# Performance work log

Measured on AMD Instinct MI355X. Metric: run time of the kernel, lower is better.

The kernel has to match this reference:

```python
import jax, jax.numpy as jnp
import numpy as np

N_NODES = 100000


def setup_inputs() -> dict:
    key = jax.random.key(0)
    k1, k2, k3, k4, k5 = jax.random.split(key, 5)
    feature = jax.random.normal(k1, (N_NODES, 64), dtype=jnp.float32)
    src = jax.random.randint(k2, (1600000,), 0, N_NODES, dtype=jnp.int64)
    dst = jax.random.randint(k3, (1600000,), 0, N_NODES, dtype=jnp.int64)
    W = jax.random.normal(k4, (64, 64), dtype=jnp.float32) * 0.1  # [in_feats, out_feats]
    b = jax.random.normal(k5, (64,), dtype=jnp.float32) * 0.1
    return {"feature": feature, "src": src, "dst": dst, "W": W, "b": b}


def reference(feature, src, dst, W, b):
    # message: m_e = h[src_e]; reduce: mean over mailbox per dst node.
    msgs = feature[src]                                   # [E, d] gather
    summed = jax.ops.segment_sum(msgs, dst, num_segments=N_NODES)  # [N, d]
    ones = jnp.ones((dst.shape[0],), dtype=feature.dtype)
    deg = jax.ops.segment_sum(ones, dst, num_segments=N_NODES)    # [N]
    mean = summed / jnp.maximum(deg, 1.0)[:, None]
    # DGL: nodes with no incoming messages keep their original feature
    h = jnp.where((deg > 0)[:, None], mean, feature)
    # apply_nodes: ReLU(W h + b)
    out = jax.nn.relu(h @ W + b)
    return out
```

## Files before the change

kernel.cpp:

```cpp
#include <hip/hip_runtime.h>
#include <hip/hip_bf16.h>

#define D 64
#define LOGB 7
#define BNODES 128
#define GRP6 32
#define CH6 1024
#define TN 64

__device__ __forceinline__ float blo(unsigned u) { return __uint_as_float(u << 16); }
__device__ __forceinline__ float bhi(unsigned u) { return __uint_as_float(u & 0xffff0000u); }
__device__ __forceinline__ ushort f2bfr(float x) {
    __hip_bfloat16 hb = __float2bfloat16(x);
    return *reinterpret_cast<ushort*>(&hb);
}


__global__ __launch_bounds__(256) void k_hist(
    const int* __restrict__ dst, int* __restrict__ cnt, int n_edges, int nbkt)
{
    __shared__ int sc[1024];
    int t = threadIdx.x;
    for (int i = t; i < 1024; i += 256) sc[i] = 0;
    __syncthreads();
    int n4 = n_edges >> 2;
    const int4* d4 = (const int4*)dst;
    int stride = gridDim.x * 256;
    for (int i = blockIdx.x * 256 + t; i < n4; i += stride) {
        int4 d = d4[i];
        atomicAdd(&sc[d.x >> LOGB], 1);
        atomicAdd(&sc[d.y >> LOGB], 1);
        atomicAdd(&sc[d.z >> LOGB], 1);
        atomicAdd(&sc[d.w >> LOGB], 1);
    }
    if (blockIdx.x == 0 && t == 0)
        for (int e = n4 << 2; e < n_edges; ++e) atomicAdd(&cnt[dst[e] >> LOGB], 1);
    __syncthreads();
    for (int i = t; i < nbkt; i += 256) {
        int c = sc[i];
        if (c) atomicAdd(&cnt[i], c);
    }
}


__global__ __launch_bounds__(1024) void k_bin_scan(
    const int* __restrict__ cnt, int* __restrict__ base,
    int* __restrict__ cursor, int nbkt)
{
    int t = threadIdx.x;
    int v = (t < nbkt) ? cnt[t] : 0;
    int lane = t & 63;
    int incl = v;
    #pragma unroll
    for (int o = 1; o < 64; o <<= 1) {
        int u = __shfl_up(incl, o, 64);
        if (lane >= o) incl += u;
    }
    __shared__ int wtot[16];
    if (lane == 63) wtot[t >> 6] = incl;
    __syncthreads();
    int wpre = 0;
    int w = t >> 6;
    for (int i = 0; i < w; ++i) wpre += wtot[i];
    int excl = wpre + incl - v;
    if (t < nbkt) { base[t] = excl; cursor[t] = excl; }
    if (t == nbkt - 1) base[nbkt] = excl + v;
}


__global__ __launch_bounds__(256) void k_fused(
    const int* __restrict__ src, const int* __restrict__ dst,
    int* __restrict__ cursor, unsigned* __restrict__ packed,
    int n_edges, int sbits, int nblk,
    const float* __restrict__ feat, const float* __restrict__ W,
    ushort* __restrict__ g, int n_nodes)
{
    __shared__ __align__(16) char smem[45072];
    int t = threadIdx.x;

    if ((int)blockIdx.x < nblk) {
        int* s_cnt  = (int*)smem;
        int* s_base = (int*)(smem + 4096);
        int* s_gb   = (int*)(smem + 8192);
        int* wtot   = (int*)(smem + 12288);
        unsigned* s_stage = (unsigned*)(smem + 12304);
        int* s_addr = (int*)(smem + 28688);

        int chbase = blockIdx.x * 4096;
        int count = n_edges - chbase;
        if (count > 4096) count = 4096;

        for (int i = t; i < 1024; i += 256) s_cnt[i] = 0;
        __syncthreads();

        #pragma unroll
        for (int k = 0; k < 16; ++k) {
            int i = t + k * 256;
            if (i < count) atomicAdd(&s_cnt[dst[chbase + i] >> LOGB], 1);
        }
        __syncthreads();

        int b4 = t * 4;
        int v0 = s_cnt[b4], v1 = s_cnt[b4 + 1], v2 = s_cnt[b4 + 2], v3 = s_cnt[b4 + 3];
        int ssum = v0 + v1 + v2 + v3;
        int lane = t & 63;
        int incl = ssum;
        #pragma unroll
        for (int o = 1; o < 64; o <<= 1) {
            int u = __shfl_up(incl, o, 64);
            if (lane >= o) incl += u;
        }
        if (lane == 63) wtot[t >> 6] = incl;
        __syncthreads();
        int wpre = 0;
        int w = t >> 6;
        for (int i = 0; i < w; ++i) wpre += wtot[i];
        int excl = wpre + incl - ssum;
        s_base[b4]     = excl;
        s_base[b4 + 1] = excl + v0;
        s_base[b4 + 2] = excl + v0 + v1;
        s_base[b4 + 3] = excl + v0 + v1 + v2;
        __syncthreads();

        for (int i = t; i < 1024; i += 256) {
            int c = s_cnt[i];
            s_gb[i] = c ? atomicAdd(&cursor[i], c) : 0;
        }
        __syncthreads();
        for (int i = t; i < 1024; i += 256) s_cnt[i] = s_base[i];
        __syncthreads();

        #pragma unroll
        for (int k = 0; k < 16; ++k) {
            int i = t + k * 256;
            if (i < count) {
                int e = chbase + i;
                int d = dst[e];
                int s = src[e];
                int bkt = d >> LOGB;
                int pos = atomicAdd(&s_cnt[bkt], 1);
                s_stage[pos] = ((unsigned)(d & (BNODES - 1)) << sbits) | (unsigned)s;
                s_addr[pos]  = s_gb[bkt] + (pos - s_base[bkt]);
            }
        }
        __syncthreads();

        #pragma unroll
        for (int k = 0; k < 16; ++k) {
            int i = t + k * 256;
            if (i < count) packed[s_addr[i]] = s_stage[i];
        }
    } else {
        float* ft = (float*)smem;
        float* Ws = (float*)(smem + 16384);

        int bid = blockIdx.x - nblk;
        int n0 = bid * TN;

        if (bid == 0 && t < 64) g[(size_t)n_nodes * D + t] = 0;

        {
            const float4* W4 = (const float4*)W;
            float4* Ws4 = (float4*)Ws;
            #pragma unroll
            for (int i = 0; i < 4; ++i) Ws4[t + i * 256] = W4[t + i * 256];
        }
        {
            const float4* f4 = (const float4*)feat;
            #pragma unroll
            for (int it = 0; it < 4; ++it) {
                int i = it * 256 + t;
                int r = i >> 4, c = i & 15;
                int node = n0 + r;
                float4 v = (node < n_nodes) ? f4[(size_t)node * 16 + c]
                                            : make_float4(0.f, 0.f, 0.f, 0.f);
                ft[(4 * c + 0) * TN + r] = v.x;
                ft[(4 * c + 1) * TN + r] = v.y;
                ft[(4 * c + 2) * TN + r] = v.z;
                ft[(4 * c + 3) * TN + r] = v.w;
            }
        }
        __syncthreads();

        int nq = t >> 4, cq = t & 15;
        int n4 = nq * 4, c4 = cq * 4;

        float4 a0 = make_float4(0.f, 0.f, 0.f, 0.f);
        float4 a1 = a0, a2 = a0, a3 = a0;

        #pragma unroll 16
        for (int k = 0; k < D; ++k) {
            float4 fv = *reinterpret_cast<const float4*>(&ft[k * TN + n4]);
            float4 wv = *reinterpret_cast<const float4*>(&Ws[k * D + c4]);
            a0.x = fmaf(fv.x, wv.x, a0.x); a0.y = fmaf(fv.x, wv.y, a0.y);
            a0.z = fmaf(fv.x, wv.z, a0.z); a0.w = fmaf(fv.x, wv.w, a0.w);
            a1.x = fmaf(fv.y, wv.x, a1.x); a1.y = fmaf(fv.y, wv.y, a1.y);
            a1.z = fmaf(fv.y, wv.z, a1.z); a1.w = fmaf(fv.y, wv.w, a1.w);
            a2.x = fmaf(fv.z, wv.x, a2.x); a2.y = fmaf(fv.z, wv.y, a2.y);
            a2.z = fmaf(fv.z, wv.z, a2.z); a2.w = fmaf(fv.z, wv.w, a2.w);
            a3.x = fmaf(fv.w, wv.x, a3.x); a3.y = fmaf(fv.w, wv.y, a3.y);
            a3.z = fmaf(fv.w, wv.z, a3.z); a3.w = fmaf(fv.w, wv.w, a3.w);
        }

        float4 accs[4] = {a0, a1, a2, a3};
        #pragma unroll
        for (int i = 0; i < 4; ++i) {
            int node = n0 + n4 + i;
            if (node < n_nodes) {
                ushort4 o;
                o.x = f2bfr(accs[i].x);
                o.y = f2bfr(accs[i].y);
                o.z = f2bfr(accs[i].z);
                o.w = f2bfr(accs[i].w);
                *reinterpret_cast<ushort4*>(g + (size_t)node * D + c4) = o;
            }
        }
    }
}


__global__ __launch_bounds__(256) void k_sort128(
    const unsigned* __restrict__ packed,
    const int* __restrict__ bbase,
    int* __restrict__ csr2,
    int* __restrict__ noff,
    int n_nodes, int sbits)
{
    __shared__ int s_cnt[BNODES];
    __shared__ int s_off[BNODES + 1];

    int t = threadIdx.x;
    int b = blockIdx.x;
    int gb = bbase[b], cnt = bbase[b + 1] - gb;

    if (t < BNODES) s_cnt[t] = 0;
    __syncthreads();
    for (int i = t; i < cnt; i += 256)
        atomicAdd(&s_cnt[packed[gb + i] >> sbits], 1);
    __syncthreads();

    if (t < 64) {
        int v0 = s_cnt[2 * t], v1 = s_cnt[2 * t + 1];
        int s = v0 + v1, incl = s;
        #pragma unroll
        for (int o = 1; o < 64; o <<= 1) {
            int u = __shfl_up(incl, o, 64);
            if (t >= o) incl += u;
        }
        int excl = incl - s;
        s_off[2 * t] = excl;
        s_off[2 * t + 1] = excl + v0;
        if (t == 63) s_off[BNODES] = incl;
    }
    __syncthreads();

    if (t <= BNODES) {
        int node = b * BNODES + t;
        if (node <= n_nodes) noff[node] = gb + s_off[t];
    }
    if (t < BNODES) s_cnt[t] = s_off[t];
    __syncthreads();

    unsigned smask = (1u << sbits) - 1u;
    for (int i = t; i < cnt; i += 256) {
        unsigned v = packed[gb + i];
        int pos = atomicAdd(&s_cnt[v >> sbits], 1);
        csr2[gb + pos] = (int)(v & smask);
    }
}


__global__ __launch_bounds__(256) void k_bucket6(
    const ushort* __restrict__ g,
    const float* __restrict__ bias,
    const int* __restrict__ noff,
    const int* __restrict__ csr2,
    float* __restrict__ out, int n_nodes)
{
    __shared__ int s_src[CH6];
    __shared__ int s_noff[GRP6 + 1];

    int t = threadIdx.x;
    int n0 = blockIdx.x * GRP6;
    if (t <= GRP6) {
        int node = n0 + t;
        s_noff[t] = noff[node > n_nodes ? n_nodes : node];
    }
    __syncthreads();

    int lane = t & 63, wid = t >> 6;
    int q = lane >> 4;
    int m = lane & 15;
    const ushort* gm = g + 4 * m;

    float4 acc[8];
    #pragma unroll
    for (int k = 0; k < 8; ++k) acc[k] = make_float4(0.f, 0.f, 0.f, 0.f);

    int beg = s_noff[0], end = s_noff[GRP6];
    for (int cb = beg; cb < end; cb += CH6) {
        int ce = cb + CH6 < end ? cb + CH6 : end;
        __syncthreads();
        for (int i = cb + t; i < ce; i += 256) s_src[i - cb] = csr2[i];
        __syncthreads();

        #pragma unroll
        for (int k = 0; k < 8; ++k) {
            int r = wid * 8 + k;
            int lo = s_noff[r], hi = s_noff[r + 1];
            if (lo < cb) lo = cb;
            if (hi > ce) hi = ce;
            float4 a = acc[k];
            for (int i = lo; i < hi; i += 16) {
                int i0 = i + q, i1 = i0 + 4, i2 = i0 + 8, i3 = i0 + 12;
                int s0 = (i0 < hi) ? s_src[i0 - cb] : n_nodes;
                int s1 = (i1 < hi) ? s_src[i1 - cb] : n_nodes;
                int s2 = (i2 < hi) ? s_src[i2 - cb] : n_nodes;
                int s3 = (i3 < hi) ? s_src[i3 - cb] : n_nodes;
                uint2 u0 = *reinterpret_cast<const uint2*>(gm + (size_t)s0 * D);
                uint2 u1 = *reinterpret_cast<const uint2*>(gm + (size_t)s1 * D);
                uint2 u2 = *reinterpret_cast<const uint2*>(gm + (size_t)s2 * D);
                uint2 u3 = *reinterpret_cast<const uint2*>(gm + (size_t)s3 * D);
                a.x += blo(u0.x); a.y += bhi(u0.x); a.z += blo(u0.y); a.w += bhi(u0.y);
                a.x += blo(u1.x); a.y += bhi(u1.x); a.z += blo(u1.y); a.w += bhi(u1.y);
                a.x += blo(u2.x); a.y += bhi(u2.x); a.z += blo(u2.y); a.w += bhi(u2.y);
                a.x += blo(u3.x); a.y += bhi(u3.x); a.z += blo(u3.y); a.w += bhi(u3.y);
            }
            acc[k] = a;
        }
    }

    float4 bj = *reinterpret_cast<const float4*>(bias + 4 * m);
    #pragma unroll
    for (int k = 0; k < 8; ++k) {
        float4 v = acc[k];
        v.x += __shfl_xor(v.x, 16, 64);
        v.y += __shfl_xor(v.y, 16, 64);
        v.z += __shfl_xor(v.z, 16, 64);
        v.w += __shfl_xor(v.w, 16, 64);
        v.x += __shfl_xor(v.x, 32, 64);
        v.y += __shfl_xor(v.y, 32, 64);
        v.z += __shfl_xor(v.z, 32, 64);
        v.w += __shfl_xor(v.w, 32, 64);
        if ((k & 3) == q) {
            int r = wid * 8 + k;
            int node = n0 + r;
            if (node < n_nodes) {
                int dgt = s_noff[r + 1] - s_noff[r];
                float4 res;
                if (dgt > 0) {
                    float inv = 1.0f / (float)dgt;
                    res = make_float4(v.x * inv, v.y * inv, v.z * inv, v.w * inv);
                } else {
                    uint2 u = *reinterpret_cast<const uint2*>(gm + (size_t)node * D);
                    res = make_float4(blo(u.x), bhi(u.x), blo(u.y), bhi(u.y));
                }
                res.x = fmaxf(res.x + bj.x, 0.0f);
                res.y = fmaxf(res.y + bj.y, 0.0f);
                res.z = fmaxf(res.z + bj.z, 0.0f);
                res.w = fmaxf(res.w + bj.w, 0.0f);
                *reinterpret_cast<float4*>(out + (size_t)node * D + 4 * m) = res;
            }
        }
    }
}


extern "C" void kernel_launch(void* const* d_in, const int* in_sizes, int n_in,
                              void* d_out, int out_size, void* d_ws, size_t ws_size,
                              hipStream_t stream)
{
    const float* feat = (const float*)d_in[0];
    const int*   src  = (const int*)d_in[1];
    const int*   dst  = (const int*)d_in[2];
    const float* W    = (const float*)d_in[3];
    const float* b    = (const float*)d_in[4];
    float* out = (float*)d_out;

    int n_nodes = in_sizes[0] / D;
    int n_edges = in_sizes[1];
    int nbkt = (n_nodes + BNODES - 1) >> LOGB;

    int sbits = 1;
    while ((1 << sbits) < n_nodes && sbits < 25) sbits++;

    size_t base_off   = 0;
    size_t cnt_off    = (((size_t)(nbkt + 1) * 4) + 63) & ~(size_t)63;
    size_t cursor_off = (cnt_off + (size_t)nbkt * 4 + 63) & ~(size_t)63;
    size_t noff_off   = (cursor_off + (size_t)nbkt * 4 + 63) & ~(size_t)63;
    size_t packed_off = (noff_off + ((size_t)n_nodes + 1) * 4 + 63) & ~(size_t)63;
    size_t csr2_off   = (packed_off + (size_t)n_edges * 4 + 63) & ~(size_t)63;
    size_t g_off      = (csr2_off + (size_t)n_edges * 4 + 63) & ~(size_t)63;
    size_t need       = g_off + ((size_t)n_nodes + 1) * D * 2;

    bool ok = (ws_size >= need) && (nbkt <= 1024) && (sbits + LOGB <= 32) &&
              ((1 << sbits) >= n_nodes);
    if (!ok) return;

    char* ws = (char*)d_ws;
    int* bbase   = (int*)(ws + base_off);
    int* bcnt    = (int*)(ws + cnt_off);
    int* bcursor = (int*)(ws + cursor_off);
    int* noff    = (int*)(ws + noff_off);
    unsigned* packed = (unsigned*)(ws + packed_off);
    int* csr2    = (int*)(ws + csr2_off);
    ushort* g    = (ushort*)(ws + g_off);

    int tblk = (n_nodes + TN - 1) / TN;
    int nblk = (n_edges + 4095) / 4096;

    hipMemsetAsync(bcnt, 0, (size_t)nbkt * 4, stream);
    k_hist<<<256, 256, 0, stream>>>(dst, bcnt, n_edges, nbkt);
    k_bin_scan<<<1, 1024, 0, stream>>>(bcnt, bbase, bcursor, nbkt);
    k_fused<<<nblk + tblk, 256, 0, stream>>>(src, dst, bcursor, packed,
                                             n_edges, sbits, nblk,
                                             feat, W, g, n_nodes);
    k_sort128<<<nbkt, 256, 0, stream>>>(packed, bbase, csr2, noff,
                                        n_nodes, sbits);
    int ngrp6 = (n_nodes + GRP6 - 1) / GRP6;
    k_bucket6<<<ngrp6, 256, 0, stream>>>(g, b, noff, csr2, out, n_nodes);
}
```

Measured before the change: 100.1 us.

## Interleave scatter and GEMM blocks, swizzle feature tile, replace memset kernel

Interleaves scatter blocks evenly among the node-transform blocks in the fused launch, one scatter block every R blocks, so both kinds of work are spread across CUs at the same time instead of all scatter blocks dispatching first. It also XOR-swizzles the transposed feature tile in shared memory to reduce bank conflicts on the transposed writes, and swaps hipMemsetAsync for a small zeroing kernel. The cost is extra index arithmetic per block. The swizzle mapping must stay consistent between the writes and the float4 reads.

```diff
diff --git a/kernel.cpp b/kernel.cpp
--- a/kernel.cpp
+++ b/kernel.cpp
@@ -13,6 +13,13 @@
 __device__ __forceinline__ ushort f2bfr(float x) {
     __hip_bfloat16 hb = __float2bfloat16(x);
     return *reinterpret_cast<ushort*>(&hb);
+}
+
+
+__global__ __launch_bounds__(256) void k_zero(int* __restrict__ p, int n)
+{
+    int i = blockIdx.x * 256 + threadIdx.x;
+    if (i < n) p[i] = 0;
 }
 
 
@@ -71,14 +78,17 @@
 __global__ __launch_bounds__(256) void k_fused(
     const int* __restrict__ src, const int* __restrict__ dst,
     int* __restrict__ cursor, unsigned* __restrict__ packed,
-    int n_edges, int sbits, int nblk,
+    int n_edges, int sbits, int nblk, int R,
     const float* __restrict__ feat, const float* __restrict__ W,
     ushort* __restrict__ g, int n_nodes)
 {
     __shared__ __align__(16) char smem[45072];
     int t = threadIdx.x;
-
-    if ((int)blockIdx.x < nblk) {
+    int bid = (int)blockIdx.x;
+    int sidx = bid / R;
+    bool is_scatter = ((bid % R) == 0) && (sidx < nblk);
+
+    if (is_scatter) {
         int* s_cnt  = (int*)smem;
         int* s_base = (int*)(smem + 4096);
         int* s_gb   = (int*)(smem + 8192);
@@ -86,7 +96,7 @@
         unsigned* s_stage = (unsigned*)(smem + 12304);
         int* s_addr = (int*)(smem + 28688);
 
-        int chbase = blockIdx.x * 4096;
+        int chbase = sidx * 4096;
         int count = n_edges - chbase;
         if (count > 4096) count = 4096;
 
@@ -154,10 +164,10 @@
         float* ft = (float*)smem;
         float* Ws = (float*)(smem + 16384);
 
-        int bid = blockIdx.x - nblk;
-        int n0 = bid * TN;
-
-        if (bid == 0 && t < 64) g[(size_t)n_nodes * D + t] = 0;
+        int tid = bid - min(nblk, (bid + R - 1) / R);
+        int n0 = tid * TN;
+
+        if (tid == 0 && t < 64) g[(size_t)n_nodes * D + t] = 0;
 
         {
             const float4* W4 = (const float4*)W;
@@ -174,10 +184,11 @@
                 int node = n0 + r;
                 float4 v = (node < n_nodes) ? f4[(size_t)node * 16 + c]
                                             : make_float4(0.f, 0.f, 0.f, 0.f);
-                ft[(4 * c + 0) * TN + r] = v.x;
-                ft[(4 * c + 1) * TN + r] = v.y;
-                ft[(4 * c + 2) * TN + r] = v.z;
-                ft[(4 * c + 3) * TN + r] = v.w;
+                int sw = r ^ (4 * c);
+                ft[(4 * c + 0) * 64 + sw] = v.x;
+                ft[(4 * c + 1) * 64 + sw] = v.y;
+                ft[(4 * c + 2) * 64 + sw] = v.z;
+                ft[(4 * c + 3) * 64 + sw] = v.w;
             }
         }
         __syncthreads();
@@ -190,7 +201,7 @@
 
         #pragma unroll 16
         for (int k = 0; k < D; ++k) {
-            float4 fv = *reinterpret_cast<const float4*>(&ft[k * TN + n4]);
+            float4 fv = *reinterpret_cast<const float4*>(&ft[k * 64 + (n4 ^ (k & 60))]);
             float4 wv = *reinterpret_cast<const float4*>(&Ws[k * D + c4]);
             a0.x = fmaf(fv.x, wv.x, a0.x); a0.y = fmaf(fv.x, wv.y, a0.y);
             a0.z = fmaf(fv.x, wv.z, a0.z); a0.w = fmaf(fv.x, wv.w, a0.w);
@@ -408,13 +419,15 @@
 
     int tblk = (n_nodes + TN - 1) / TN;
     int nblk = (n_edges + 4095) / 4096;
-
-    hipMemsetAsync(bcnt, 0, (size_t)nbkt * 4, stream);
+    int grid = nblk + tblk;
+    int R = grid / nblk;
+
+    k_zero<<<(nbkt + 255) / 256, 256, 0, stream>>>(bcnt, nbkt);
     k_hist<<<256, 256, 0, stream>>>(dst, bcnt, n_edges, nbkt);
     k_bin_scan<<<1, 1024, 0, stream>>>(bcnt, bbase, bcursor, nbkt);
-    k_fused<<<nblk + tblk, 256, 0, stream>>>(src, dst, bcursor, packed,
-                                             n_edges, sbits, nblk,
-                                             feat, W, g, n_nodes);
+    k_fused<<<grid, 256, 0, stream>>>(src, dst, bcursor, packed,
+                                      n_edges, sbits, nblk, R,
+                                      feat, W, g, n_nodes);
     k_sort128<<<nbkt, 256, 0, stream>>>(packed, bbase, csr2, noff,
                                         n_nodes, sbits);
     int ngrp6 = (n_nodes + GRP6 - 1) / GRP6;
```

Result: slower. 117.1 us (+17.0%).
